# Kernel optimization log

Hardware: AMD Instinct MI355X
Metric: run time of the kernel (lower is better)

Reference implementation:

```python
import jax, jax.numpy as jnp
import numpy as np

B, S, D = 4, 2048, 1024

def setup_inputs() -> dict:
    key = jax.random.key(0)
    kx, kk, kq, kv = jax.random.split(key, 4)
    scale = 1.0 / np.sqrt(D)
    x = jax.random.normal(kx, (B, S, D), dtype=jnp.float32)
    # nn.Linear weights, applied as x @ W.T; init with small scale like torch default
    Wk = jax.random.normal(kk, (D, D), dtype=jnp.float32) * scale
    Wq = jax.random.normal(kq, (D, D), dtype=jnp.float32) * scale
    Wv = jax.random.normal(kv, (D, D), dtype=jnp.float32) * scale
    return {"x": x, "Wk": Wk, "Wq": Wq, "Wv": Wv}

def reference(x, Wk, Wq, Wv):
    # k/q/v: (B, S, D) @ (D, D_out) -- Linear applies W as x @ W.T
    k = jnp.einsum('bsd,kd->bsk', x, Wk)
    q = jnp.einsum('bsd,kd->bsk', x, Wq)
    v = jnp.einsum('bsd,vd->bsv', x, Wv)
    # scaled dot-product scores: (B, S, S)
    scores = jnp.einsum('bqk,bsk->bqs', q, k) / jnp.sqrt(jnp.asarray(k.shape[-1], x.dtype))
    # causal mask: allow j <= i (upper-right masked out)
    S_len = x.shape[1]
    causal = jnp.tril(jnp.ones((S_len, S_len), dtype=bool))
    scores = jnp.where(causal[None, :, :], scores, jnp.asarray(-jnp.inf, x.dtype))
    weights = jax.nn.softmax(scores, axis=-1)
    # dropout is identity in eval / p used as deterministic baseline
    out = jnp.einsum('bqs,bsv->bqv', weights, v)
    return out
```

## Files before the change

### kernel.cpp

```cpp
#include <hip/hip_runtime.h>

typedef __attribute__((ext_vector_type(8))) short bf16x8;
typedef __attribute__((ext_vector_type(4))) float f32x4;
typedef __attribute__((ext_vector_type(4))) unsigned short u16x4;
typedef __attribute__((ext_vector_type(8))) unsigned short u16x8;

#define MFMA16(a, b, c) __builtin_amdgcn_mfma_f32_16x16x32_bf16((a), (b), (c), 0, 0, 0)

__device__ __forceinline__ ushort f2bf(float f) {
    unsigned u = __float_as_uint(f);
    unsigned r = (u + 0x7FFFu + ((u >> 16) & 1u)) >> 16;
    return (ushort)r;
}
__device__ __forceinline__ float bf2f(ushort s) {
    return __uint_as_float(((unsigned)s) << 16);
}

__device__ __forceinline__ void async16(const ushort* g, ushort* l) {
    __builtin_amdgcn_global_load_lds(
        (const __attribute__((address_space(1))) unsigned*)g,
        (__attribute__((address_space(3))) unsigned*)l, 16, 0, 0);
}

#define SBAR()  __builtin_amdgcn_s_barrier()
#define SCHED() __builtin_amdgcn_sched_barrier(0)

__global__ __launch_bounds__(256) void cvt_all(
    const float* __restrict__ x,  const float* __restrict__ wk,
    const float* __restrict__ wq, const float* __restrict__ wv,
    ushort* __restrict__ xb,  ushort* __restrict__ wvb,
    ushort* __restrict__ wkt, ushort* __restrict__ wqt)
{
    __shared__ float t[32][33];
    int bx = blockIdx.x;
    if (bx < 4608) {
        const size_t XN = (size_t)8192 * 1024;
        size_t idx = ((size_t)bx * 256 + threadIdx.x) * 8;
        const float* s;
        ushort* d;
        if (idx < XN) { s = x + idx; d = xb + idx; }
        else          { s = wv + (idx - XN); d = wvb + (idx - XN); }
        float4 a = *(const float4*)s;
        float4 b = *(const float4*)(s + 4);
        u16x8 p;
        p[0] = f2bf(a.x); p[1] = f2bf(a.y); p[2] = f2bf(a.z); p[3] = f2bf(a.w);
        p[4] = f2bf(b.x); p[5] = f2bf(b.y); p[6] = f2bf(b.z); p[7] = f2bf(b.w);
        *(u16x8*)d = p;
    } else {
        bx -= 4608;
        const int z  = bx >> 10;
        const int tb = bx & 1023;
        const int e0 = (tb & 31) * 32, d0 = (tb >> 5) * 32;
        const float* src = z ? wq : wk;
        ushort*      dst = z ? wqt : wkt;
        const int tx = threadIdx.x & 31, ty = threadIdx.x >> 5;
#pragma unroll
        for (int r = 0; r < 4; ++r)
            t[ty + 8 * r][tx] = src[(size_t)(e0 + ty + 8 * r) * 1024 + d0 + tx];
        __syncthreads();
#pragma unroll
        for (int r = 0; r < 4; ++r)
            dst[(size_t)(d0 + ty + 8 * r) * 1024 + e0 + tx] = f2bf(t[tx][ty + 8 * r]);
    }
}

__device__ __forceinline__ void mma_tile(
    const ushort* __restrict__ A, int lda, int abase,
    const ushort* __restrict__ B, int ldb, int bbase,
    int ktiles,
    ushort* As, ushort* Bs, f32x4 (&acc)[4][4])
{
    const int tid  = threadIdx.x;
    const int lane = tid & 63, wid = tid >> 6;
    const int wr = wid >> 1, wc = wid & 1;
    const int lrow = lane & 15, kgrp = lane >> 4;
    const int ci = lane >> 3;
    const int cc = (lane & 7) * 8;

#pragma unroll
    for (int m = 0; m < 4; ++m)
#pragma unroll
        for (int n = 0; n < 4; ++n) acc[m][n] = (f32x4){0.f, 0.f, 0.f, 0.f};

    for (int kt = 0; kt < ktiles; ++kt) {
        const int k0 = kt * 64;
#pragma unroll
        for (int i = 0; i < 4; ++i) {
            const int r = (wid * 4 + i) * 8 + ci;
            async16(&A[(size_t)(abase + r) * lda + k0 + cc], &As[(wid * 4 + i) * 512]);
            async16(&B[(size_t)(bbase + r) * ldb + k0 + cc], &Bs[(wid * 4 + i) * 512]);
        }
        __syncthreads();
#pragma unroll
        for (int kk = 0; kk < 2; ++kk) {
            bf16x8 af[4], bfr[4];
#pragma unroll
            for (int m = 0; m < 4; ++m)
                af[m] = *(const bf16x8*)&As[(wr * 64 + m * 16 + lrow) * 64 + kk * 32 + kgrp * 8];
#pragma unroll
            for (int n = 0; n < 4; ++n)
                bfr[n] = *(const bf16x8*)&Bs[(wc * 64 + n * 16 + lrow) * 64 + kk * 32 + kgrp * 8];
#pragma unroll
            for (int m = 0; m < 4; ++m)
#pragma unroll
                for (int n = 0; n < 4; ++n)
                    acc[m][n] = MFMA16(af[m], bfr[n], acc[m][n]);
        }
        __syncthreads();
    }
}

__device__ __forceinline__ void mma256(
    const ushort* __restrict__ A, int lda, int abase,
    const ushort* __restrict__ B, int ldb, int bbase,
    int NT, ushort* As, ushort* Bs, f32x4 (&acc)[8][4])
{
    const int tid  = threadIdx.x;
    const int lane = tid & 63, w = tid >> 6;
    const int wr = w >> 2, wc = w & 3;
    const int lrow = lane & 15, kgrp = lane >> 4;
    const int sgl  = ((lane & 7) ^ ((lane >> 3) & 7)) * 8;
    const int srow = lane >> 3;

    auto stage = [&](int t, int isB, int hi) {
        const ushort* src = isB ? B : A;
        const int ld = isB ? ldb : lda;
        const int rb = isB ? bbase : abase;
        ushort* buf = (isB ? Bs : As) + (size_t)(t & 1) * 16384;
#pragma unroll
        for (int i = 0; i < 2; ++i) {
            const int r = hi * 128 + (w * 2 + i) * 8 + srow;
            async16(&src[(size_t)(rb + r) * ld + t * 64 + sgl],
                    buf + (size_t)(hi * 128 + (w * 2 + i) * 8) * 64 + lane * 8);
        }
    };

#pragma unroll
    for (int m = 0; m < 8; ++m)
#pragma unroll
        for (int n = 0; n < 4; ++n) acc[m][n] = (f32x4){0.f, 0.f, 0.f, 0.f};

    stage(0, 0, 0); stage(0, 0, 1); stage(0, 1, 0); stage(0, 1, 1);
    if (NT > 1) {
        stage(1, 0, 0); stage(1, 0, 1);
        asm volatile("s_waitcnt vmcnt(4)" ::: "memory");
    } else {
        asm volatile("s_waitcnt vmcnt(0)" ::: "memory");
    }
    SCHED();
    SBAR();
    SCHED();

    const int sw = lrow & 7;

    for (int t = 0; t < NT; ++t) {
        ushort* Ab = As + (size_t)(t & 1) * 16384;
        ushort* Bb = Bs + (size_t)(t & 1) * 16384;
        bf16x8 af[8], bfr[2];

        {
            const int g = (kgrp ^ sw) * 8;
#pragma unroll
            for (int m = 0; m < 8; ++m)
                af[m] = *(const bf16x8*)&Ab[(wr * 128 + m * 16 + lrow) * 64 + g];
#pragma unroll
            for (int n = 0; n < 2; ++n)
                bfr[n] = *(const bf16x8*)&Bb[(wc * 64 + n * 16 + lrow) * 64 + g];
        }
        if (t + 1 < NT) stage(t + 1, 1, 0);
        SBAR(); SCHED();
        __builtin_amdgcn_s_setprio(1);
#pragma unroll
        for (int m = 0; m < 8; ++m) {
            acc[m][0] = MFMA16(af[m], bfr[0], acc[m][0]);
            acc[m][1] = MFMA16(af[m], bfr[1], acc[m][1]);
        }
        __builtin_amdgcn_s_setprio(0);
        SBAR(); SCHED();

        {
            const int g = (kgrp ^ sw) * 8;
#pragma unroll
            for (int n = 0; n < 2; ++n)
                bfr[n] = *(const bf16x8*)&Bb[(wc * 64 + (2 + n) * 16 + lrow) * 64 + g];
        }
        if (t + 1 < NT) stage(t + 1, 1, 1);
        SBAR(); SCHED();
        __builtin_amdgcn_s_setprio(1);
#pragma unroll
        for (int m = 0; m < 8; ++m) {
            acc[m][2] = MFMA16(af[m], bfr[0], acc[m][2]);
            acc[m][3] = MFMA16(af[m], bfr[1], acc[m][3]);
        }
        __builtin_amdgcn_s_setprio(0);
        SBAR(); SCHED();

        {
            const int g = ((4 + kgrp) ^ sw) * 8;
#pragma unroll
            for (int m = 0; m < 8; ++m)
                af[m] = *(const bf16x8*)&Ab[(wr * 128 + m * 16 + lrow) * 64 + g];
#pragma unroll
            for (int n = 0; n < 2; ++n)
                bfr[n] = *(const bf16x8*)&Bb[(wc * 64 + n * 16 + lrow) * 64 + g];
        }
        SBAR(); SCHED();
        __builtin_amdgcn_s_setprio(1);
#pragma unroll
        for (int m = 0; m < 8; ++m) {
            acc[m][0] = MFMA16(af[m], bfr[0], acc[m][0]);
            acc[m][1] = MFMA16(af[m], bfr[1], acc[m][1]);
        }
        __builtin_amdgcn_s_setprio(0);
        SBAR(); SCHED();

        {
            const int g = ((4 + kgrp) ^ sw) * 8;
#pragma unroll
            for (int n = 0; n < 2; ++n)
                bfr[n] = *(const bf16x8*)&Bb[(wc * 64 + (2 + n) * 16 + lrow) * 64 + g];
        }
        if (t + 2 < NT) {
            stage(t + 2, 0, 0); stage(t + 2, 0, 1);
            asm volatile("s_waitcnt vmcnt(4)" ::: "memory");
        } else if (t + 1 < NT) {
            asm volatile("s_waitcnt vmcnt(0)" ::: "memory");
        }
        SCHED();
        SBAR(); SCHED();
        __builtin_amdgcn_s_setprio(1);
#pragma unroll
        for (int m = 0; m < 8; ++m) {
            acc[m][2] = MFMA16(af[m], bfr[0], acc[m][2]);
            acc[m][3] = MFMA16(af[m], bfr[1], acc[m][3]);
        }
        __builtin_amdgcn_s_setprio(0);
        SBAR(); SCHED();
    }
}

__global__ __launch_bounds__(256) void m_gemm(
    const ushort* __restrict__ Wkt, const ushort* __restrict__ Wqt,
    ushort* __restrict__ Mtr)
{
    __shared__ ushort As[128 * 64];
    __shared__ ushort Bs[128 * 64];
    const int fbase = blockIdx.x * 128;
    const int dbase = blockIdx.y * 128;

    f32x4 acc[4][4];
    mma_tile(Wkt, 1024, fbase, Wqt, 1024, dbase, 16, As, Bs, acc);

    const int lane = threadIdx.x & 63, wid = threadIdx.x >> 6;
    const int wr = wid >> 1, wc = wid & 1;
    const int lrow = lane & 15, kgrp = lane >> 4;
#pragma unroll
    for (int m = 0; m < 4; ++m)
#pragma unroll
        for (int n = 0; n < 4; ++n)
#pragma unroll
            for (int r = 0; r < 4; ++r) {
                const int gf = fbase + wr * 64 + m * 16 + kgrp * 4 + r;
                const int gd = dbase + wc * 64 + n * 16 + lrow;
                Mtr[(size_t)gf * 1024 + gd] = f2bf(acc[m][n][r] * 0.03125f);
            }
}

__global__ __launch_bounds__(512, 2) void tv_gemm8(
    const ushort* __restrict__ xb, const ushort* __restrict__ Mtr,
    const ushort* __restrict__ Wvb,
    ushort* __restrict__ Tb, ushort* __restrict__ Vt)
{
    __shared__ ushort As[2 * 16384];
    __shared__ ushort Bs[2 * 16384];

    const int z = blockIdx.z;
    const ushort* Bmat = z ? Wvb : Mtr;
    const int mbase = blockIdx.x * 256;
    const int nbase = blockIdx.y * 256;

    f32x4 acc[8][4];
    mma256(xb, 1024, mbase, Bmat, 1024, nbase, 16, As, Bs, acc);

    const int lane = threadIdx.x & 63, w = threadIdx.x >> 6;
    const int wr = w >> 2, wc = w & 3;
    const int lrow = lane & 15, kgrp = lane >> 4;

    if (z == 1) {
        const int b  = mbase >> 11;
        const int s0 = mbase & 2047;
        ushort* VtB = Vt + (size_t)b * 1024 * 2048;
#pragma unroll
        for (int m = 0; m < 8; ++m)
#pragma unroll
            for (int n = 0; n < 4; ++n) {
                u16x4 pk;
#pragma unroll
                for (int r = 0; r < 4; ++r) pk[r] = f2bf(acc[m][n][r]);
                const int d = nbase + wc * 64 + n * 16 + lrow;
                const int s = s0 + wr * 128 + m * 16 + kgrp * 4;
                *(u16x4*)&VtB[(size_t)d * 2048 + s] = pk;
            }
    } else {
#pragma unroll
        for (int m = 0; m < 8; ++m)
#pragma unroll
            for (int n = 0; n < 4; ++n)
#pragma unroll
                for (int r = 0; r < 4; ++r) {
                    const int gr = mbase + wr * 128 + m * 16 + kgrp * 4 + r;
                    const int gc = nbase + wc * 64 + n * 16 + lrow;
                    Tb[(size_t)gr * 1024 + gc] = f2bf(acc[m][n][r]);
                }
    }
}

__global__ __launch_bounds__(512, 2) void scores_gemm8(
    const ushort* __restrict__ Tb, const ushort* __restrict__ xb,
    ushort* __restrict__ Sall)
{
    __shared__ ushort As[2 * 16384];
    __shared__ ushort Bs[2 * 16384];

    ushort* S = Sall + (size_t)blockIdx.y * 2048 * 2048;
    const int rb = blockIdx.y * 2048;

    int t = blockIdx.x;
    int it = (int)((sqrtf(8.0f * (float)t + 1.0f) - 1.0f) * 0.5f);
    while ((it + 1) * (it + 2) / 2 <= t) ++it;
    while (it * (it + 1) / 2 > t) --it;
    const int jt = t - it * (it + 1) / 2;
    const int ibase = it * 256, jbase = jt * 256;
    const bool diag = (it == jt);

    f32x4 acc[8][4];
    mma256(Tb, 1024, rb + ibase, xb, 1024, rb + jbase, 16, As, Bs, acc);

    const int lane = threadIdx.x & 63, w = threadIdx.x >> 6;
    const int wr = w >> 2, wc = w & 3;
    const int lrow = lane & 15, kgrp = lane >> 4;
#pragma unroll
    for (int m = 0; m < 8; ++m)
#pragma unroll
        for (int n = 0; n < 4; ++n)
#pragma unroll
            for (int r = 0; r < 4; ++r) {
                const int gi = ibase + wr * 128 + m * 16 + kgrp * 4 + r;
                const int gj = jbase + wc * 64 + n * 16 + lrow;
                float p = __expf(acc[m][n][r]);
                if (diag && gj > gi) p = 0.f;
                S[(size_t)gi * 2048 + gj] = f2bf(p);
            }
}

__device__ __forceinline__ void pv_sub(
    const ushort* __restrict__ P, const ushort* __restrict__ Vt,
    float* __restrict__ O, int it, int nbase,
    ushort* As, ushort* Bs, float* rs)
{
    const int tid  = threadIdx.x;
    const int lane = tid & 63, w = tid >> 6;
    const int wr = w >> 2, wc = w & 3;
    const int lrow = lane & 15, kgrp = lane >> 4;
    const int srow = lane >> 3;
    const int sc16 = (lane & 7) ^ srow;
    const int pbase = it * 128;
    const int NT = 2 * (it + 1);

    auto stage = [&](int t) {
        ushort* dA = As + (size_t)(t & 1) * 8192;
        ushort* dB = Bs + (size_t)(t & 1) * 8192;
#pragma unroll
        for (int i = 0; i < 2; ++i) {
            const int rr = (i * 8 + w) * 8 + srow;
            async16(&P [(size_t)(pbase + rr) * 2048 + t * 64 + sc16 * 8],
                    dA + ((i * 8 + w) * 64 + lane) * 8);
            async16(&Vt[(size_t)(nbase + rr) * 2048 + t * 64 + sc16 * 8],
                    dB + ((i * 8 + w) * 64 + lane) * 8);
        }
    };

    f32x4 acc[4][2];
#pragma unroll
    for (int m = 0; m < 4; ++m)
#pragma unroll
        for (int n = 0; n < 2; ++n) acc[m][n] = (f32x4){0.f, 0.f, 0.f, 0.f};
    float fs = 0.f;

    stage(0);
    if (NT > 1) { stage(1); asm volatile("s_waitcnt vmcnt(4)" ::: "memory"); }
    else        {           asm volatile("s_waitcnt vmcnt(0)" ::: "memory"); }
    SCHED();
    SBAR(); SCHED();

    for (int t = 0; t < NT; ++t) {
        const ushort* Ab = As + (size_t)(t & 1) * 8192;
        const ushort* Bb = Bs + (size_t)(t & 1) * 8192;
        bf16x8 af[2][4], bq[2][2];
#pragma unroll
        for (int kk = 0; kk < 2; ++kk) {
            const int p16 = (kk * 4 + kgrp) ^ (lrow & 7);
#pragma unroll
            for (int m = 0; m < 4; ++m) {
                const int row = wr * 64 + m * 16 + lrow;
                af[kk][m] = *(const bf16x8*)&Ab[row * 64 + p16 * 8];
            }
#pragma unroll
            for (int n = 0; n < 2; ++n) {
                const int row = wc * 32 + n * 16 + lrow;
                bq[kk][n] = *(const bf16x8*)&Bb[row * 64 + p16 * 8];
            }
        }
        asm volatile("s_waitcnt lgkmcnt(0)" ::: "memory");
        SCHED();
#pragma unroll
        for (int kk = 0; kk < 2; ++kk)
#pragma unroll
            for (int m = 0; m < 4; ++m)
                if (m == wc) {
#pragma unroll
                    for (int e = 0; e < 8; ++e)
                        fs += bf2f((ushort)af[kk][m][e]);
                }
        SBAR(); SCHED();
        if (t + 2 < NT) {
            stage(t + 2);
            asm volatile("s_waitcnt vmcnt(4)" ::: "memory");
        } else if (t + 1 < NT) {
            asm volatile("s_waitcnt vmcnt(0)" ::: "memory");
        }
        SCHED();
        SBAR(); SCHED();
        __builtin_amdgcn_s_setprio(1);
#pragma unroll
        for (int kk = 0; kk < 2; ++kk)
#pragma unroll
            for (int m = 0; m < 4; ++m) {
                acc[m][0] = MFMA16(af[kk][m], bq[kk][0], acc[m][0]);
                acc[m][1] = MFMA16(af[kk][m], bq[kk][1], acc[m][1]);
            }
        __builtin_amdgcn_s_setprio(0);
    }

    fs += __shfl_xor(fs, 16);
    fs += __shfl_xor(fs, 32);
    if (lane < 16) rs[wr * 64 + wc * 16 + lane] = fs;
    __syncthreads();

#pragma unroll
    for (int m = 0; m < 4; ++m)
#pragma unroll
        for (int r = 0; r < 4; ++r) {
            const int ri = wr * 64 + m * 16 + kgrp * 4 + r;
            const float inv = 1.0f / rs[ri];
            const int gi = pbase + ri;
#pragma unroll
            for (int n = 0; n < 2; ++n) {
                const int gc = nbase + wc * 32 + n * 16 + lrow;
                O[(size_t)gi * 1024 + gc] = acc[m][n][r] * inv;
            }
        }
    __syncthreads();
}

__global__ __launch_bounds__(512, 2) void pv_pair(
    const ushort* __restrict__ Pall, const ushort* __restrict__ Vtall,
    float* __restrict__ Oall)
{
    __shared__ ushort As[2 * 8192];
    __shared__ ushort Bs[2 * 8192];
    __shared__ float rs[128];

    const ushort* P  = Pall  + (size_t)blockIdx.z * 2048 * 2048;
    const ushort* Vt = Vtall + (size_t)blockIdx.z * 1024 * 2048;
    float*        O  = Oall  + (size_t)blockIdx.z * 2048 * 1024;
    const int nbase = blockIdx.y * 128;

    pv_sub(P, Vt, O, 15 - (int)blockIdx.x, nbase, As, Bs, rs);
    pv_sub(P, Vt, O, (int)blockIdx.x,      nbase, As, Bs, rs);
}

extern "C" void kernel_launch(void* const* d_in, const int* in_sizes, int n_in,
                              void* d_out, int out_size, void* d_ws, size_t ws_size,
                              hipStream_t stream)
{
    (void)in_sizes; (void)n_in; (void)out_size; (void)ws_size;
    const float* x  = (const float*)d_in[0];
    const float* Wk = (const float*)d_in[1];
    const float* Wq = (const float*)d_in[2];
    const float* Wv = (const float*)d_in[3];
    float* out = (float*)d_out;

    const size_t M1 = (size_t)1024 * 1024;
    ushort* ws  = (ushort*)d_ws;
    ushort* xb  = ws;
    ushort* Tb  = xb  + 8 * M1;
    ushort* Vt  = Tb  + 8 * M1;
    ushort* Sb  = Vt  + 8 * M1;
    ushort* Wkt = Sb  + 16 * M1;
    ushort* Wqt = Wkt + M1;
    ushort* Wvb = Wqt + M1;
    ushort* Mtr = Wvb + M1;

    cvt_all<<<6656, 256, 0, stream>>>(x, Wk, Wq, Wv, xb, Wvb, Wkt, Wqt);
    m_gemm<<<dim3(8, 8), 256, 0, stream>>>(Wkt, Wqt, Mtr);
    tv_gemm8<<<dim3(32, 4, 2), 512, 0, stream>>>(xb, Mtr, Wvb, Tb, Vt);
    scores_gemm8<<<dim3(36, 4), 512, 0, stream>>>(Tb, xb, Sb);
    pv_pair<<<dim3(8, 8, 4), 512, 0, stream>>>(Sb, Vt, out);
}
```

Measured before the change: 150.5 us.

## Compute softmax row sums in scores kernel and triple-buffer PV staging

The scores kernel now reduces exp values per row within each 256x256 tile and writes partial row sums to a workspace buffer. The PV kernel reads and sums these partials instead of accumulating bf16 P values inside its main loop. The PV loop also moves from double to triple-buffered LDS staging with a prefetch distance of three. This removes per-iteration summation work and deepens the memory pipeline, at the cost of more LDS per block (possibly affecting occupancy) and an extra reduction plus store in the scores epilogue. Row sums now come from fp32 p before bf16 rounding, which slightly changes the normalisation numerics.

Result: no change. 149.2 us (-0.9%).

```diff
diff --git a/kernel.cpp b/kernel.cpp
--- a/kernel.cpp
+++ b/kernel.cpp
@@ -317,7 +317,7 @@
 
 __global__ __launch_bounds__(512, 2) void scores_gemm8(
     const ushort* __restrict__ Tb, const ushort* __restrict__ xb,
-    ushort* __restrict__ Sall)
+    ushort* __restrict__ Sall, float* __restrict__ rsum)
 {
     __shared__ ushort As[2 * 16384];
     __shared__ ushort Bs[2 * 16384];
@@ -336,9 +336,17 @@
     f32x4 acc[8][4];
     mma256(Tb, 1024, rb + ibase, xb, 1024, rb + jbase, 16, As, Bs, acc);
 
-    const int lane = threadIdx.x & 63, w = threadIdx.x >> 6;
+    const int tid = threadIdx.x;
+    const int lane = tid & 63, w = tid >> 6;
     const int wr = w >> 2, wc = w & 3;
     const int lrow = lane & 15, kgrp = lane >> 4;
+
+    float prs[8][4];
+#pragma unroll
+    for (int m = 0; m < 8; ++m)
+#pragma unroll
+        for (int r = 0; r < 4; ++r) prs[m][r] = 0.f;
+
 #pragma unroll
     for (int m = 0; m < 8; ++m)
 #pragma unroll
@@ -350,13 +358,41 @@
                 float p = __expf(acc[m][n][r]);
                 if (diag && gj > gi) p = 0.f;
                 S[(size_t)gi * 2048 + gj] = f2bf(p);
-            }
+                prs[m][r] += p;
+            }
+
+    float* psum = (float*)As;
+#pragma unroll
+    for (int m = 0; m < 8; ++m)
+#pragma unroll
+        for (int r = 0; r < 4; ++r) {
+            float v = prs[m][r];
+            v += __shfl_xor(v, 1);
+            v += __shfl_xor(v, 2);
+            v += __shfl_xor(v, 4);
+            v += __shfl_xor(v, 8);
+            prs[m][r] = v;
+        }
+    if (lrow == 0) {
+#pragma unroll
+        for (int m = 0; m < 8; ++m)
+#pragma unroll
+            for (int r = 0; r < 4; ++r)
+                psum[(wr * 4 + wc) * 128 + m * 16 + kgrp * 4 + r] = prs[m][r];
+    }
+    __syncthreads();
+    if (tid < 256) {
+        const int half = tid >> 7, rr = tid & 127;
+        float s4 = psum[(half * 4 + 0) * 128 + rr] + psum[(half * 4 + 1) * 128 + rr]
+                 + psum[(half * 4 + 2) * 128 + rr] + psum[(half * 4 + 3) * 128 + rr];
+        rsum[(size_t)(blockIdx.y * 9 + jt) * 2048 + ibase + tid] = s4;
+    }
 }
 
 __device__ __forceinline__ void pv_sub(
     const ushort* __restrict__ P, const ushort* __restrict__ Vt,
-    float* __restrict__ O, int it, int nbase,
-    ushort* As, ushort* Bs, float* rs)
+    float* __restrict__ O, const float* __restrict__ rsb,
+    int it, int nbase, ushort* As, ushort* Bs, float* rs)
 {
     const int tid  = threadIdx.x;
     const int lane = tid & 63, w = tid >> 6;
@@ -366,10 +402,11 @@
     const int sc16 = (lane & 7) ^ srow;
     const int pbase = it * 128;
     const int NT = 2 * (it + 1);
-
-    auto stage = [&](int t) {
-        ushort* dA = As + (size_t)(t & 1) * 8192;
-        ushort* dB = Bs + (size_t)(t & 1) * 8192;
+    const int jtmax = it >> 1;
+
+    auto stage = [&](int t, int slot) {
+        ushort* dA = As + (size_t)slot * 8192;
+        ushort* dB = Bs + (size_t)slot * 8192;
 #pragma unroll
         for (int i = 0; i < 2; ++i) {
             const int rr = (i * 8 + w) * 8 + srow;
@@ -380,22 +417,34 @@
         }
     };
 
+    if (tid < 128) {
+        float s = 0.f;
+        for (int j = 0; j <= jtmax; ++j)
+            s += rsb[(size_t)j * 2048 + pbase + tid];
+        rs[tid] = 1.0f / s;
+    }
+
     f32x4 acc[4][2];
 #pragma unroll
     for (int m = 0; m < 4; ++m)
 #pragma unroll
         for (int n = 0; n < 2; ++n) acc[m][n] = (f32x4){0.f, 0.f, 0.f, 0.f};
-    float fs = 0.f;
-
-    stage(0);
-    if (NT > 1) { stage(1); asm volatile("s_waitcnt vmcnt(4)" ::: "memory"); }
-    else        {           asm volatile("s_waitcnt vmcnt(0)" ::: "memory"); }
+
+    stage(0, 0);
+    if (NT > 2) {
+        stage(1, 1); stage(2, 2);
+        asm volatile("s_waitcnt vmcnt(8)" ::: "memory");
+    } else {
+        stage(1, 1);
+        asm volatile("s_waitcnt vmcnt(4)" ::: "memory");
+    }
     SCHED();
     SBAR(); SCHED();
 
+    int bi = 0;
     for (int t = 0; t < NT; ++t) {
-        const ushort* Ab = As + (size_t)(t & 1) * 8192;
-        const ushort* Bb = Bs + (size_t)(t & 1) * 8192;
+        const ushort* Ab = As + (size_t)bi * 8192;
+        const ushort* Bb = Bs + (size_t)bi * 8192;
         bf16x8 af[2][4], bq[2][2];
 #pragma unroll
         for (int kk = 0; kk < 2; ++kk) {
@@ -413,20 +462,13 @@
         }
         asm volatile("s_waitcnt lgkmcnt(0)" ::: "memory");
         SCHED();
-#pragma unroll
-        for (int kk = 0; kk < 2; ++kk)
-#pragma unroll
-            for (int m = 0; m < 4; ++m)
-                if (m == wc) {
-#pragma unroll
-                    for (int e = 0; e < 8; ++e)
-                        fs += bf2f((ushort)af[kk][m][e]);
-                }
-        SBAR(); SCHED();
-        if (t + 2 < NT) {
-            stage(t + 2);
+        SBAR(); SCHED();
+        if (t + 3 < NT) {
+            stage(t + 3, bi);
+            asm volatile("s_waitcnt vmcnt(8)" ::: "memory");
+        } else if (t + 3 == NT) {
             asm volatile("s_waitcnt vmcnt(4)" ::: "memory");
-        } else if (t + 1 < NT) {
+        } else if (t + 2 == NT) {
             asm volatile("s_waitcnt vmcnt(0)" ::: "memory");
         }
         SCHED();
@@ -440,11 +482,9 @@
                 acc[m][1] = MFMA16(af[kk][m], bq[kk][1], acc[m][1]);
             }
         __builtin_amdgcn_s_setprio(0);
-    }
-
-    fs += __shfl_xor(fs, 16);
-    fs += __shfl_xor(fs, 32);
-    if (lane < 16) rs[wr * 64 + wc * 16 + lane] = fs;
+        bi = (bi == 2) ? 0 : bi + 1;
+    }
+
     __syncthreads();
 
 #pragma unroll
@@ -452,7 +492,7 @@
 #pragma unroll
         for (int r = 0; r < 4; ++r) {
             const int ri = wr * 64 + m * 16 + kgrp * 4 + r;
-            const float inv = 1.0f / rs[ri];
+            const float inv = rs[ri];
             const int gi = pbase + ri;
 #pragma unroll
             for (int n = 0; n < 2; ++n) {
@@ -465,19 +505,20 @@
 
 __global__ __launch_bounds__(512, 2) void pv_pair(
     const ushort* __restrict__ Pall, const ushort* __restrict__ Vtall,
-    float* __restrict__ Oall)
-{
-    __shared__ ushort As[2 * 8192];
-    __shared__ ushort Bs[2 * 8192];
+    const float* __restrict__ rsum, float* __restrict__ Oall)
+{
+    __shared__ ushort As[3 * 8192];
+    __shared__ ushort Bs[3 * 8192];
     __shared__ float rs[128];
 
     const ushort* P  = Pall  + (size_t)blockIdx.z * 2048 * 2048;
     const ushort* Vt = Vtall + (size_t)blockIdx.z * 1024 * 2048;
+    const float* rsb = rsum  + (size_t)blockIdx.z * 9 * 2048;
     float*        O  = Oall  + (size_t)blockIdx.z * 2048 * 1024;
     const int nbase = blockIdx.y * 128;
 
-    pv_sub(P, Vt, O, 15 - (int)blockIdx.x, nbase, As, Bs, rs);
-    pv_sub(P, Vt, O, (int)blockIdx.x,      nbase, As, Bs, rs);
+    pv_sub(P, Vt, O, rsb, 15 - (int)blockIdx.x, nbase, As, Bs, rs);
+    pv_sub(P, Vt, O, rsb, (int)blockIdx.x,      nbase, As, Bs, rs);
 }
 
 extern "C" void kernel_launch(void* const* d_in, const int* in_sizes, int n_in,
@@ -501,10 +542,11 @@
     ushort* Wqt = Wkt + M1;
     ushort* Wvb = Wqt + M1;
     ushort* Mtr = Wvb + M1;
+    float*  rsum = (float*)(Mtr + M1);
 
     cvt_all<<<6656, 256, 0, stream>>>(x, Wk, Wq, Wv, xb, Wvb, Wkt, Wqt);
     m_gemm<<<dim3(8, 8), 256, 0, stream>>>(Wkt, Wqt, Mtr);
     tv_gemm8<<<dim3(32, 4, 2), 512, 0, stream>>>(xb, Mtr, Wvb, Tb, Vt);
-    scores_gemm8<<<dim3(36, 4), 512, 0, stream>>>(Tb, xb, Sb);
-    pv_pair<<<dim3(8, 8, 4), 512, 0, stream>>>(Sb, Vt, out);
-}
+    scores_gemm8<<<dim3(36, 4), 512, 0, stream>>>(Tb, xb, Sb, rsum);
+    pv_pair<<<dim3(8, 8, 4), 512, 0, stream>>>(Sb, Vt, rsum, out);
+}
```
